# Performance work log

Measured on AMD Instinct MI355X. Metric: run time of the kernel, lower is better.

Reference implementation:

```python
import jax, jax.numpy as jnp
import numpy as np

# Config (mirrors CorrLayerDownsample(J=3, L=8, A=1, A_prime=1, M=256, N=256,
# num_channels=1, shift_mode='samec', mask_angles=4)). With samec + 1 channel,
# every pair is 'shifted' (mask index 1) and groups (j1,j2) are contiguous in
# the global moment order, so concatenation reproduces results_storage order.
J, L, A, M, N, NB = 3, 8, 1, 256, 256, 2
MASK_ANGLES = 4
RADII = (1, 2)  # dyadic shift radii (assumed form of create_masks_shift)

def _mask_positions():
    # shift mask 1: origin plus shifts along mask_angles directions at dyadic radii
    pos = {(0, 0)}
    for k in range(MASK_ANGLES):
        th = np.pi * k / MASK_ANGLES
        for r in RADII:
            pos.add((int(round(r * np.cos(th))), int(round(r * np.sin(th)))))
    return sorted(pos)

def _union_flat_idx(h, w):
    # row-major flat indices of the union shift mask at resolution (h, w),
    # matching torch boolean-mask indexing order (mask_downsample + mask_idx_map_1)
    return np.array(sorted(((dx % h) * w + (dy % w)) for dx, dy in _mask_positions()), dtype=np.int64)

UNION_IDX = [_union_flat_idx(M >> j, N >> j) for j in range(J)]
NSHIFT = len(UNION_IDX[0])

# per-(j1,j2) channel gather indices: la = A*L*c + A*l + a = l (A=1, c=0)
# loop order in compute_idx: l1 outer, l2 inner
LA1 = np.repeat(np.arange(L), L)
LA2 = np.tile(np.arange(L), L)

def _spectral_pad(xh, Mn, Nn):
    # zero-pad Fourier representation to (Mn, Nn) -- spectral upsampling
    m, n = xh.shape[-2], xh.shape[-1]
    if (m, n) == (Mn, Nn):
        return xh
    xs = jnp.fft.fftshift(xh, axes=(-2, -1))
    ph, pw = (Mn - m) // 2, (Nn - n) // 2
    pad = [(0, 0)] * (xh.ndim - 2) + [(ph, ph), (pw, pw)]
    xp = jnp.pad(xs, pad)
    return jnp.fft.ifftshift(xp, axes=(-2, -1)) * ((Mn * Nn) / (m * n))

def _forward(xpsi_0, xpsi_1, xpsi_2):
    xs = [xpsi_0, xpsi_1, xpsi_2]
    hats = [jnp.fft.fft2(x.astype(jnp.complex64)) for x in xs]  # [nb, C, h_j, w_j]
    la1 = jnp.asarray(LA1)
    la2 = jnp.asarray(LA2)
    outs = []
    for j1 in range(J):
        h, w = M >> j1, N >> j1
        uidx = jnp.asarray(UNION_IDX[j1])
        h1 = hats[j1][:, la1]  # [nb, P=L*L, h, w]
        for j2 in range(j1, J):
            h2 = hats[j2][:, la2]
            if j2 > j1:
                h2 = _spectral_pad(h2, h, w)  # upsample coarser scale to scale j1
            corr = jnp.fft.ifft2(h1 * jnp.conj(h2)).real  # cross-correlation map
            flat = corr.reshape(corr.shape[0], corr.shape[1], h * w)
            outs.append(flat[:, :, uidx])  # masked downsample: keep shift positions
    return jnp.concatenate(outs, axis=1)  # [nb, total_pairs, NSHIFT]

def setup_inputs():
    key = jax.random.key(0)
    ks = jax.random.split(key, 3)
    return {
        "xpsi_0": jax.random.normal(ks[0], (NB, A * L, M, N), dtype=jnp.float32),
        "xpsi_1": jax.random.normal(ks[1], (NB, A * L, M // 2, N // 2), dtype=jnp.float32),
        "xpsi_2": jax.random.normal(ks[2], (NB, A * L, M // 4, N // 4), dtype=jnp.float32),
    }

def reference(xpsi_0, xpsi_1, xpsi_2):
    return _forward(xpsi_0, xpsi_1, xpsi_2)
```

## Files before the change

kernel.cpp:

```cpp
#include <hip/hip_runtime.h>

#define PI_D 3.14159265358979323846
#define PI_F 3.14159265358979323846f


__device__ inline float rtab_val(int n, int m2, int t) {
  if (t == 0) return 1.0f;
  double th = PI_D * (double)t / (double)n;
  double v = sin(th * (double)(m2 - 1)) / sin(th) + cos(th * (double)m2);
  return (float)(v / (double)m2);
}

__global__ __launch_bounds__(256) void k_front(const float* __restrict__ X1,
                                               const float* __restrict__ X2,
                                               float* __restrict__ P1p,
                                               float* __restrict__ P2p,
                                               float* __restrict__ V01,
                                               float* __restrict__ V02,
                                               float* __restrict__ V12,
                                               float* __restrict__ out) {
  int bid = blockIdx.x;
  int t = threadIdx.x;
  if (bid == 640) {
    for (int i = t; i < 5376; i += 256) out[i] = 0.f;
    return;
  }
  if (bid < 192) {
    const float* X; float* P; int lg, nsp, idx0;
    if (bid < 128) { X = X1; P = P1p; lg = 7; nsp = 8; idx0 = bid; }
    else           { X = X2; P = P2p; lg = 6; nsp = 4; idx0 = bid - 128; }
    int ch = idx0 / nsp, split = idx0 % nsp;
    int n = 1 << lg;
    int total = n * n;
    int chunk = total / nsp;
    int b0 = split * chunk;
    const float* x = X + (size_t)ch * total + b0;
    float s = 0.f;
    for (int i = t; i < chunk; i += 256) {
      int idx = b0 + i;
      float v = x[i];
      s += (((idx >> lg) ^ idx) & 1) ? -v : v;
    }
#pragma unroll
    for (int off = 32; off > 0; off >>= 1) s += __shfl_down(s, off, 64);
    __shared__ float red[4];
    if ((t & 63) == 0) red[t >> 6] = s;
    __syncthreads();
    if (t == 0) P[ch * nsp + split] = red[0] + red[1] + red[2] + red[3];
    return;
  }
  int vbid = bid - 192;
  const float* X; float* V;
  int n1, n2, s, ch, nxg, colh;
  if (vbid < 256) {
    X = X1; V = V01; n1 = 256; n2 = 128; s = 2;
    ch = vbid >> 4; nxg = ((vbid >> 1) & 7) * 16; colh = vbid & 1;
  } else if (vbid < 384) {
    int w = vbid - 256;
    X = X2; V = V02; n1 = 256; n2 = 64; s = 4;
    ch = w >> 3; nxg = ((w >> 1) & 3) * 16; colh = w & 1;
  } else {
    int w = vbid - 384;
    X = X2; V = V12; n1 = 128; n2 = 64; s = 2;
    ch = w >> 2; nxg = (w & 3) * 16; colh = 0;
  }
  __shared__ float Rl[256];
  __shared__ float Xs[16 * 128];
  for (int i = t; i < n1; i += 256) Rl[i] = rtab_val(n1, n2, i);
  const float4* xch4 =
      (const float4*)(X + (size_t)ch * n2 * n2 + (size_t)nxg * n2);
  int nx4 = (16 * n2) >> 2;
  for (int i = t; i < nx4; i += 256) ((float4*)Xs)[i] = xch4[i];
  __syncthreads();
  int myq = (t & 63) + colh * 128;
  int nxq = t >> 6;
  int mask = n1 - 1;
  float acc[4][2];
#pragma unroll
  for (int r = 0; r < 4; ++r)
#pragma unroll
    for (int c = 0; c < 2; ++c) acc[r][c] = 0.f;
  for (int ny = 0; ny < n2; ++ny) {
    float xv[4];
#pragma unroll
    for (int r = 0; r < 4; ++r) xv[r] = Xs[(4 * nxq + r) * n2 + ny];
#pragma unroll
    for (int c = 0; c < 2; ++c) {
      float rv = Rl[(myq + 64 * c - s * ny) & mask];
#pragma unroll
      for (int r = 0; r < 4; ++r) acc[r][c] += xv[r] * rv;
    }
  }
  float* vch = V + (size_t)ch * n2 * n1;
#pragma unroll
  for (int r = 0; r < 4; ++r)
    for (int c = 0; c < 2; ++c)
      vch[(size_t)(nxg + 4 * nxq + r) * n1 + myq + 64 * c] = acc[r][c];
}

__global__ __launch_bounds__(256) void k_main(const float* __restrict__ X0,
                                              const float* __restrict__ X1,
                                              const float* __restrict__ X2,
                                              const float* __restrict__ V01,
                                              const float* __restrict__ V02,
                                              const float* __restrict__ V12,
                                              const float* __restrict__ P1p,
                                              const float* __restrict__ P2p,
                                              float* __restrict__ out) {
  __shared__ float sRl[256];
  __shared__ float4 R4[256];
  __shared__ float sh[4864];
  int u = blockIdx.x;
  int t = threadIdx.x;
  int lane = t & 63;
  int wv = t >> 6;

  float accC[8][7];
#pragma unroll
  for (int i = 0; i < 8; ++i)
#pragma unroll
    for (int p = 0; p < 7; ++p) accC[i][p] = 0.f;

  int base, b, l2;

  if (u < 640) {
    const float* V; const float* Pp; const float* A1b;
    int n1, n2, s, ch, chunk, nsp, lgn1; float inv;
    if (u < 256)      { V = V01; Pp = P1p; nsp = 8; A1b = X0; n1 = 256; n2 = 128; s = 2; inv = 1.f / (128.f * 128.f); ch = u >> 4; chunk = u & 15; lgn1 = 8; base = 64; }
    else if (u < 512) { int w = u - 256; V = V02; Pp = P2p; nsp = 4; A1b = X0; n1 = 256; n2 = 64; s = 4; inv = 1.f / (64.f * 64.f); ch = w >> 4; chunk = w & 15; lgn1 = 8; base = 128; }
    else              { int w = u - 512; V = V12; Pp = P2p; nsp = 4; A1b = X1; n1 = 128; n2 = 64; s = 2; inv = 1.f / (64.f * 64.f); ch = w >> 3; chunk = w & 7; lgn1 = 7; base = 256; }
    int mask = n1 - 1;
    for (int i = t; i < n1; i += 256) sRl[i] = rtab_val(n1, n2, i);
    __syncthreads();
    for (int i = t; i < n1; i += 256)
      R4[i] = make_float4(sRl[i], sRl[(i + 1) & mask], sRl[(i + 2) & mask],
                          sRl[(i + 3) & mask]);
    __syncthreads();
    int mxg = chunk * 16;
    b = ch >> 3; l2 = ch & 7;
    const float* vch = V + (size_t)ch * n2 * n1;
    float Pv = 0.f;
    for (int i = 0; i < nsp; ++i) Pv += Pp[ch * nsp + i];
    float a = PI_F / (float)s;
    int per = 2 * s;
    if (n1 == 256) {
      int cid = t & 63;
      int rb = mxg - 2 + 5 * wv;
      float4 acc[5];
#pragma unroll
      for (int j = 0; j < 5; ++j) acc[j] = make_float4(0.f, 0.f, 0.f, 0.f);
      float4 vv = *(const float4*)(vch + 4 * cid);
      for (int nx = 0; nx < n2; ++nx) {
        float4 vvn;
        if (nx + 1 < n2) vvn = *(const float4*)(vch + (size_t)(nx + 1) * 256 + 4 * cid);
        int ib = (rb - s * nx) & mask;
        float4 r03 = R4[ib];
        float r4v = sRl[(ib + 4) & mask];
        float rv[5] = {r03.x, r03.y, r03.z, r03.w, r4v};
#pragma unroll
        for (int j = 0; j < 5; ++j) {
          acc[j].x += rv[j] * vv.x; acc[j].y += rv[j] * vv.y;
          acc[j].z += rv[j] * vv.z; acc[j].w += rv[j] * vv.w;
        }
        vv = vvn;
      }
      float smy[4];
#pragma unroll
      for (int j = 0; j < 4; ++j) smy[j] = sinf(a * (float)((4 * cid + j) & (per - 1)));
#pragma unroll
      for (int j = 0; j < 5; ++j) {
        int rl = 5 * wv + j;
        if (rl < 19) {
          int mx = (mxg - 2 + rl) & mask;
          float q = inv * sinf(a * (float)(mx & (per - 1))) * Pv;
          float4 o = acc[j];
          o.x -= q * smy[0]; o.y -= q * smy[1]; o.z -= q * smy[2]; o.w -= q * smy[3];
          *(float4*)&sh[rl * 256 + 4 * cid] = o;
        }
      }
    } else {
      int cid = t & 31;
      int owner = t >> 5;
      int rb = mxg - 2 + 3 * owner;
      float4 acc[3];
#pragma unroll
      for (int j = 0; j < 3; ++j) acc[j] = make_float4(0.f, 0.f, 0.f, 0.f);
      float4 vv = *(const float4*)(vch + 4 * cid);
      for (int nx = 0; nx < 64; ++nx) {
        float4 vvn;
        if (nx + 1 < 64) vvn = *(const float4*)(vch + (size_t)(nx + 1) * 128 + 4 * cid);
        int ib = (rb - 2 * nx) & 127;
        float4 r03 = R4[ib];
        float rv[3] = {r03.x, r03.y, r03.z};
#pragma unroll
        for (int j = 0; j < 3; ++j) {
          acc[j].x += rv[j] * vv.x; acc[j].y += rv[j] * vv.y;
          acc[j].z += rv[j] * vv.z; acc[j].w += rv[j] * vv.w;
        }
        vv = vvn;
      }
      float smy[4];
#pragma unroll
      for (int j = 0; j < 4; ++j) smy[j] = sinf(a * (float)((4 * cid + j) & 3));
#pragma unroll
      for (int j = 0; j < 3; ++j) {
        int rl = 3 * owner + j;
        if (rl < 19) {
          int mx = (mxg - 2 + rl) & 127;
          float q = inv * sinf(a * (float)(mx & 3)) * Pv;
          float4 o = acc[j];
          o.x -= q * smy[0]; o.y -= q * smy[1]; o.z -= q * smy[2]; o.w -= q * smy[3];
          *(float4*)&sh[rl * 128 + 4 * cid] = o;
        }
      }
    }
    __syncthreads();
    int lgtpr = lgn1 - 2;
    int tpr = 1 << lgtpr;
    int rif = 256 >> lgtpr;
    int rid = t >> lgtpr;
    int cid2 = t & (tpr - 1);
    int ty = cid2 * 4;
    int tym = (ty - 4) & mask;
    int n1sq = n1 * n1;
    const float* A1 = A1b + (size_t)(b * 8) * n1sq;
    for (int rr = 0; rr < 16; rr += rif) {
      int ri = rr + rid;
      const float* r0 = &sh[(ri + 2) * n1];
      const float* r1 = &sh[(ri + 1) * n1];
      const float* r2 = &sh[ri * n1];
      const float* r3 = &sh[(ri + 3) * n1];
      float4 a0 = *(const float4*)(r0 + tym);
      float4 b0 = *(const float4*)(r0 + ty);
      float4 a1 = *(const float4*)(r1 + tym);
      float4 b1 = *(const float4*)(r1 + ty);
      float4 b2 = *(const float4*)(r2 + ty);
      float4 a3 = *(const float4*)(r3 + tym);
      float4 b3 = *(const float4*)(r3 + ty);
      const float* rA = A1 + (size_t)(mxg + ri) * n1 + ty;
#pragma unroll
      for (int l1 = 0; l1 < 8; ++l1) {
        float4 xv = *(const float4*)(rA + (size_t)l1 * n1sq);
        accC[l1][0] += xv.x * b0.x + xv.y * b0.y + xv.z * b0.z + xv.w * b0.w;
        accC[l1][1] += xv.x * a0.w + xv.y * b0.x + xv.z * b0.y + xv.w * b0.z;
        accC[l1][2] += xv.x * a0.z + xv.y * a0.w + xv.z * b0.x + xv.w * b0.y;
        accC[l1][3] += xv.x * b1.x + xv.y * b1.y + xv.z * b1.z + xv.w * b1.w;
        accC[l1][4] += xv.x * a1.w + xv.y * b1.x + xv.z * b1.y + xv.w * b1.z;
        accC[l1][5] += xv.x * b2.x + xv.y * b2.y + xv.z * b2.z + xv.w * b2.w;
        accC[l1][6] += xv.x * a3.w + xv.y * b3.x + xv.z * b3.y + xv.w * b3.z;
      }
    }
  } else {
    int w = u - 640;
    const float* Ab; int loc, lgn1, lgc;
    if (w < 256)      { loc = w;       Ab = X0; lgn1 = 8; lgc = 4; base = 0;   }
    else if (w < 384) { loc = w - 256; Ab = X1; lgn1 = 7; lgc = 3; base = 192; }
    else              { loc = w - 384; Ab = X2; lgn1 = 6; lgc = 2; base = 320; }
    int n1 = 1 << lgn1;
    int mask = n1 - 1;
    int n1sq = n1 * n1;
    int chunk = loc & ((1 << lgc) - 1);
    int bl2 = loc >> lgc;
    b = bl2 >> 3; l2 = bl2 & 7;
    const float* A1 = Ab + (size_t)(b * 8) * n1sq;
    const float* A2 = Ab + (size_t)(b * 8 + l2) * n1sq;
    int lgtpr = lgn1 - 2;
    int tpr = 1 << lgtpr;
    int rif = 256 >> lgtpr;
    int rid = t >> lgtpr;
    int cid2 = t & (tpr - 1);
    int ty = cid2 * 4;
    int tym = (ty - 4) & mask;
    for (int rr = 0; rr < 16; rr += rif) {
      int row = chunk * 16 + rr + rid;
      const float* r0 = A2 + (size_t)row * n1;
      const float* r1 = A2 + (size_t)((row - 1) & mask) * n1;
      const float* r2 = A2 + (size_t)((row - 2) & mask) * n1;
      const float* r3 = A2 + (size_t)((row + 1) & mask) * n1;
      float4 a0 = *(const float4*)(r0 + tym);
      float4 b0 = *(const float4*)(r0 + ty);
      float4 a1 = *(const float4*)(r1 + tym);
      float4 b1 = *(const float4*)(r1 + ty);
      float4 b2 = *(const float4*)(r2 + ty);
      float4 a3 = *(const float4*)(r3 + tym);
      float4 b3 = *(const float4*)(r3 + ty);
      const float* rA = A1 + (size_t)row * n1 + ty;
#pragma unroll
      for (int l1 = 0; l1 < 8; ++l1) {
        float4 xv = *(const float4*)(rA + (size_t)l1 * n1sq);
        accC[l1][0] += xv.x * b0.x + xv.y * b0.y + xv.z * b0.z + xv.w * b0.w;
        accC[l1][1] += xv.x * a0.w + xv.y * b0.x + xv.z * b0.y + xv.w * b0.z;
        accC[l1][2] += xv.x * a0.z + xv.y * a0.w + xv.z * b0.x + xv.w * b0.y;
        accC[l1][3] += xv.x * b1.x + xv.y * b1.y + xv.z * b1.z + xv.w * b1.w;
        accC[l1][4] += xv.x * a1.w + xv.y * b1.x + xv.z * b1.y + xv.w * b1.z;
        accC[l1][5] += xv.x * b2.x + xv.y * b2.y + xv.z * b2.z + xv.w * b2.w;
        accC[l1][6] += xv.x * a3.w + xv.y * b3.x + xv.z * b3.y + xv.w * b3.z;
      }
    }
  }
  float* af = &accC[0][0];
#pragma unroll
  for (int j = 0; j < 56; ++j) {
    float v = af[j];
    v += __shfl_down(v, 32, 64);
    v += __shfl_down(v, 16, 64);
    af[j] = v;
  }
  __syncthreads();
  if (lane < 16) {
    float* rowp = sh + (wv * 16 + lane) * 60;
#pragma unroll
    for (int j = 0; j < 14; ++j)
      *(float4*)&rowp[4 * j] =
          make_float4(af[4 * j], af[4 * j + 1], af[4 * j + 2], af[4 * j + 3]);
  }
  __syncthreads();
  if (t < 224) {
    int v = t >> 2, q = t & 3;
    float s2 = 0.f;
#pragma unroll
    for (int i = 0; i < 16; ++i) s2 += sh[(q * 16 + i) * 60 + v];
    s2 += __shfl_down(s2, 2, 64);
    s2 += __shfl_down(s2, 1, 64);
    if (q == 0) {
      int l1o = v / 7, p = v % 7;
      atomicAdd(&out[((size_t)b * 384 + base + l1o * 8 + l2) * 7 + p], s2);
    }
  }
}

extern "C" void kernel_launch(void* const* d_in, const int* in_sizes, int n_in,
                              void* d_out, int out_size, void* d_ws, size_t ws_size,
                              hipStream_t stream) {
  const float* X0 = (const float*)d_in[0];
  const float* X1 = (const float*)d_in[1];
  const float* X2 = (const float*)d_in[2];
  float* out = (float*)d_out;
  float* ws = (float*)d_ws;

  float* V01 = ws + 2359296;
  float* V02 = ws + 2883584;
  float* V12 = ws + 3145728;
  float* P1p = ws + 3276800;
  float* P2p = ws + 3276928;

  k_front<<<641, 256, 0, stream>>>(X1, X2, P1p, P2p, V01, V02, V12, out);
  k_main<<<1088, 256, 0, stream>>>(X0, X1, X2, V01, V02, V12, P1p, P2p, out);
}
```

Baseline: 103.6 us.

## Halve row chunk per block in cross-scale path and batch V prefetch by four

Cross-scale blocks now cover 8 output rows instead of 16, doubling their count (640 to 1280) and shrinking per-thread accumulators and the halo rows computed into shared memory. The V row loads are prefetched four at a time to expose more memory-level parallelism. The aim is better occupancy and load balance across CUs. In exchange, the 4-row halo and the full V-channel pass are recomputed per block, so total redundant work and V traffic roughly double.

```diff
diff --git a/kernel.cpp b/kernel.cpp
--- a/kernel.cpp
+++ b/kernel.cpp
@@ -123,12 +123,12 @@
 
   int base, b, l2;
 
-  if (u < 640) {
+  if (u < 1280) {
     const float* V; const float* Pp; const float* A1b;
     int n1, n2, s, ch, chunk, nsp, lgn1; float inv;
-    if (u < 256)      { V = V01; Pp = P1p; nsp = 8; A1b = X0; n1 = 256; n2 = 128; s = 2; inv = 1.f / (128.f * 128.f); ch = u >> 4; chunk = u & 15; lgn1 = 8; base = 64; }
-    else if (u < 512) { int w = u - 256; V = V02; Pp = P2p; nsp = 4; A1b = X0; n1 = 256; n2 = 64; s = 4; inv = 1.f / (64.f * 64.f); ch = w >> 4; chunk = w & 15; lgn1 = 8; base = 128; }
-    else              { int w = u - 512; V = V12; Pp = P2p; nsp = 4; A1b = X1; n1 = 128; n2 = 64; s = 2; inv = 1.f / (64.f * 64.f); ch = w >> 3; chunk = w & 7; lgn1 = 7; base = 256; }
+    if (u < 512)       { V = V01; Pp = P1p; nsp = 8; A1b = X0; n1 = 256; n2 = 128; s = 2; inv = 1.f / (128.f * 128.f); ch = u >> 5; chunk = u & 31; lgn1 = 8; base = 64; }
+    else if (u < 1024) { int w = u - 512;  V = V02; Pp = P2p; nsp = 4; A1b = X0; n1 = 256; n2 = 64; s = 4; inv = 1.f / (64.f * 64.f); ch = w >> 5; chunk = w & 31; lgn1 = 8; base = 128; }
+    else               { int w = u - 1024; V = V12; Pp = P2p; nsp = 4; A1b = X1; n1 = 128; n2 = 64; s = 2; inv = 1.f / (64.f * 64.f); ch = w >> 4; chunk = w & 15; lgn1 = 7; base = 256; }
     int mask = n1 - 1;
     for (int i = t; i < n1; i += 256) sRl[i] = rtab_val(n1, n2, i);
     __syncthreads();
@@ -136,7 +136,7 @@
       R4[i] = make_float4(sRl[i], sRl[(i + 1) & mask], sRl[(i + 2) & mask],
                           sRl[(i + 3) & mask]);
     __syncthreads();
-    int mxg = chunk * 16;
+    int mxg = chunk * 8;
     b = ch >> 3; l2 = ch & 7;
     const float* vch = V + (size_t)ch * n2 * n1;
     float Pv = 0.f;
@@ -145,32 +145,44 @@
     int per = 2 * s;
     if (n1 == 256) {
       int cid = t & 63;
-      int rb = mxg - 2 + 5 * wv;
-      float4 acc[5];
-#pragma unroll
-      for (int j = 0; j < 5; ++j) acc[j] = make_float4(0.f, 0.f, 0.f, 0.f);
-      float4 vv = *(const float4*)(vch + 4 * cid);
-      for (int nx = 0; nx < n2; ++nx) {
-        float4 vvn;
-        if (nx + 1 < n2) vvn = *(const float4*)(vch + (size_t)(nx + 1) * 256 + 4 * cid);
-        int ib = (rb - s * nx) & mask;
-        float4 r03 = R4[ib];
-        float r4v = sRl[(ib + 4) & mask];
-        float rv[5] = {r03.x, r03.y, r03.z, r03.w, r4v};
-#pragma unroll
-        for (int j = 0; j < 5; ++j) {
-          acc[j].x += rv[j] * vv.x; acc[j].y += rv[j] * vv.y;
-          acc[j].z += rv[j] * vv.z; acc[j].w += rv[j] * vv.w;
-        }
-        vv = vvn;
+      int rb = mxg - 2 + 3 * wv;
+      float4 acc[3];
+#pragma unroll
+      for (int j = 0; j < 3; ++j) acc[j] = make_float4(0.f, 0.f, 0.f, 0.f);
+      float4 vb[4];
+#pragma unroll
+      for (int j = 0; j < 4; ++j)
+        vb[j] = *(const float4*)(vch + (size_t)j * 256 + 4 * cid);
+      for (int nx0 = 0; nx0 < n2; nx0 += 4) {
+        float4 cur[4];
+#pragma unroll
+        for (int j = 0; j < 4; ++j) cur[j] = vb[j];
+        if (nx0 + 4 < n2) {
+#pragma unroll
+          for (int j = 0; j < 4; ++j)
+            vb[j] = *(const float4*)(vch + (size_t)(nx0 + 4 + j) * 256 + 4 * cid);
+        }
+#pragma unroll
+        for (int k = 0; k < 4; ++k) {
+          int nx = nx0 + k;
+          float4 vv = cur[k];
+          int ib = (rb - s * nx) & mask;
+          float4 r03 = R4[ib];
+          float rv[3] = {r03.x, r03.y, r03.z};
+#pragma unroll
+          for (int j = 0; j < 3; ++j) {
+            acc[j].x += rv[j] * vv.x; acc[j].y += rv[j] * vv.y;
+            acc[j].z += rv[j] * vv.z; acc[j].w += rv[j] * vv.w;
+          }
+        }
       }
       float smy[4];
 #pragma unroll
       for (int j = 0; j < 4; ++j) smy[j] = sinf(a * (float)((4 * cid + j) & (per - 1)));
 #pragma unroll
-      for (int j = 0; j < 5; ++j) {
-        int rl = 5 * wv + j;
-        if (rl < 19) {
+      for (int j = 0; j < 3; ++j) {
+        int rl = 3 * wv + j;
+        if (rl < 11) {
           int mx = (mxg - 2 + rl) & mask;
           float q = inv * sinf(a * (float)(mx & (per - 1))) * Pv;
           float4 o = acc[j];
@@ -181,31 +193,44 @@
     } else {
       int cid = t & 31;
       int owner = t >> 5;
-      int rb = mxg - 2 + 3 * owner;
-      float4 acc[3];
-#pragma unroll
-      for (int j = 0; j < 3; ++j) acc[j] = make_float4(0.f, 0.f, 0.f, 0.f);
-      float4 vv = *(const float4*)(vch + 4 * cid);
-      for (int nx = 0; nx < 64; ++nx) {
-        float4 vvn;
-        if (nx + 1 < 64) vvn = *(const float4*)(vch + (size_t)(nx + 1) * 128 + 4 * cid);
-        int ib = (rb - 2 * nx) & 127;
-        float4 r03 = R4[ib];
-        float rv[3] = {r03.x, r03.y, r03.z};
-#pragma unroll
-        for (int j = 0; j < 3; ++j) {
-          acc[j].x += rv[j] * vv.x; acc[j].y += rv[j] * vv.y;
-          acc[j].z += rv[j] * vv.z; acc[j].w += rv[j] * vv.w;
-        }
-        vv = vvn;
+      int rb = mxg - 2 + 2 * owner;
+      float4 acc[2];
+      acc[0] = make_float4(0.f, 0.f, 0.f, 0.f);
+      acc[1] = make_float4(0.f, 0.f, 0.f, 0.f);
+      float4 vb[4];
+#pragma unroll
+      for (int j = 0; j < 4; ++j)
+        vb[j] = *(const float4*)(vch + (size_t)j * 128 + 4 * cid);
+      for (int nx0 = 0; nx0 < 64; nx0 += 4) {
+        float4 cur[4];
+#pragma unroll
+        for (int j = 0; j < 4; ++j) cur[j] = vb[j];
+        if (nx0 + 4 < 64) {
+#pragma unroll
+          for (int j = 0; j < 4; ++j)
+            vb[j] = *(const float4*)(vch + (size_t)(nx0 + 4 + j) * 128 + 4 * cid);
+        }
+#pragma unroll
+        for (int k = 0; k < 4; ++k) {
+          int nx = nx0 + k;
+          float4 vv = cur[k];
+          int ib = (rb - 2 * nx) & 127;
+          float4 r03 = R4[ib];
+          float rv[2] = {r03.x, r03.y};
+#pragma unroll
+          for (int j = 0; j < 2; ++j) {
+            acc[j].x += rv[j] * vv.x; acc[j].y += rv[j] * vv.y;
+            acc[j].z += rv[j] * vv.z; acc[j].w += rv[j] * vv.w;
+          }
+        }
       }
       float smy[4];
 #pragma unroll
       for (int j = 0; j < 4; ++j) smy[j] = sinf(a * (float)((4 * cid + j) & 3));
 #pragma unroll
-      for (int j = 0; j < 3; ++j) {
-        int rl = 3 * owner + j;
-        if (rl < 19) {
+      for (int j = 0; j < 2; ++j) {
+        int rl = 2 * owner + j;
+        if (rl < 11) {
           int mx = (mxg - 2 + rl) & 127;
           float q = inv * sinf(a * (float)(mx & 3)) * Pv;
           float4 o = acc[j];
@@ -224,7 +249,7 @@
     int tym = (ty - 4) & mask;
     int n1sq = n1 * n1;
     const float* A1 = A1b + (size_t)(b * 8) * n1sq;
-    for (int rr = 0; rr < 16; rr += rif) {
+    for (int rr = 0; rr < 8; rr += rif) {
       int ri = rr + rid;
       const float* r0 = &sh[(ri + 2) * n1];
       const float* r1 = &sh[(ri + 1) * n1];
@@ -251,7 +276,7 @@
       }
     }
   } else {
-    int w = u - 640;
+    int w = u - 1280;
     const float* Ab; int loc, lgn1, lgc;
     if (w < 256)      { loc = w;       Ab = X0; lgn1 = 8; lgc = 4; base = 0;   }
     else if (w < 384) { loc = w - 256; Ab = X1; lgn1 = 7; lgc = 3; base = 192; }
@@ -345,5 +370,5 @@
   float* P2p = ws + 3276928;
 
   k_front<<<641, 256, 0, stream>>>(X1, X2, P1p, P2p, V01, V02, V12, out);
-  k_main<<<1088, 256, 0, stream>>>(X0, X1, X2, V01, V02, V12, P1p, P2p, out);
+  k_main<<<1728, 256, 0, stream>>>(X0, X1, X2, V01, V02, V12, P1p, P2p, out);
 }
```

New measurement: 140.6 us. 35.7% more time.
